# Kernel tuning notes

Hardware: AMD Instinct MI355X
Metric: run time of the kernel (lower is better)

Reference implementation:

```python
import jax, jax.numpy as jnp
import numpy as np

N = 50000       # num_nodes
E = 1_600_000   # num_edges (avg degree 32)
F_IN, HID, F_OUT = 128, 128, 64


def setup_inputs() -> dict:
    key = jax.random.key(0)
    k0, k1, k2, k3 = jax.random.split(key, 4)
    x = jax.random.normal(k0, (1, N, F_IN), dtype=jnp.float32)
    edge_index = jax.random.randint(k1, (2, E), 0, N, dtype=jnp.int32)
    # GCNConv weights (glorot-ish scale) and zero biases
    W1 = jax.random.normal(k2, (F_IN, HID), dtype=jnp.float32) / np.float32(np.sqrt(F_IN))
    b1 = jnp.zeros((HID,), dtype=jnp.float32)
    W2 = jax.random.normal(k3, (HID, F_OUT), dtype=jnp.float32) / np.float32(np.sqrt(HID))
    b2 = jnp.zeros((F_OUT,), dtype=jnp.float32)
    return {"x": x, "edge_index": edge_index, "W1": W1, "b1": b1, "W2": W2, "b2": b2}


def _gcn_layer(h, src, dst, norm, W, b, n):
    # linear transform then symmetric-normalized scatter-add aggregation
    h = h @ W                              # [N, F_out]
    msg = h[src] * norm[:, None]           # [E+N, F_out] gathered messages
    agg = jax.ops.segment_sum(msg, dst, num_segments=n)
    return agg + b


def reference(x, edge_index, W1, b1, W2, b2):
    xn = x[0]                              # [N, F_in] node feature matrix
    n = xn.shape[0]
    src, dst = edge_index[0], edge_index[1]
    # add self-loops (GCNConv default)
    loops = jnp.arange(n, dtype=src.dtype)
    src = jnp.concatenate([src, loops])
    dst = jnp.concatenate([dst, loops])
    # symmetric normalization: deg^-1/2[src] * deg^-1/2[dst] (deg >= 1 w/ self-loops)
    deg = jax.ops.segment_sum(jnp.ones(dst.shape, dtype=xn.dtype), dst, num_segments=n)
    dinv = jax.lax.rsqrt(deg)
    norm = dinv[src] * dinv[dst]
    h = jax.nn.relu(_gcn_layer(xn, src, dst, norm, W1, b1, n))
    out = jax.nn.relu(_gcn_layer(h, src, dst, norm, W2, b2, n))
    return out
```

## Files before the change

### kernel.cpp

```cpp
#include <hip/hip_runtime.h>
#include <hip/hip_fp16.h>


#define TILE 8192
#define BIN_CAP 2560

typedef _Float16 half8 __attribute__((ext_vector_type(8)));
typedef float floatx4 __attribute__((ext_vector_type(4)));

__global__ __launch_bounds__(512) void bin_kernel(const int* __restrict__ src,
                                                  const int* __restrict__ dst, int E,
                                                  int nbins,
                                                  int* __restrict__ binCnt,
                                                  unsigned* __restrict__ recs) {
    extern __shared__ int lds[];
    int* cnt = lds;
    int* gbase = lds + nbins;
    int tid = threadIdx.x;
    for (int i = tid; i < nbins; i += 512) cnt[i] = 0;
    __syncthreads();

    int t0 = blockIdx.x * TILE;
    int tEnd = min(t0 + TILE, E);

    for (int e = t0 + tid; e < tEnd; e += 512)
        atomicAdd(&cnt[dst[e] >> 6], 1);
    __syncthreads();

    for (int i = tid; i < nbins; i += 512) {
        int c = cnt[i];
        gbase[i] = (c > 0) ? atomicAdd(&binCnt[i], c) : 0;
        cnt[i] = 0;
    }
    __syncthreads();

    for (int e = t0 + tid; e < tEnd; e += 512) {
        int d = dst[e];
        int s = src[e];
        int b = d >> 6;
        int r = atomicAdd(&cnt[b], 1);
        int g = gbase[b] + r;
        if (g < BIN_CAP)
            recs[(size_t)b * BIN_CAP + g] = ((unsigned)(d & 63) << 16) | (unsigned)s;
    }
}

__global__ __launch_bounds__(512) void sort_bins(const unsigned* __restrict__ recs,
                                                 const int* __restrict__ binCnt,
                                                 unsigned short* __restrict__ sortedG,
                                                 int* __restrict__ startG,
                                                 float* __restrict__ dinv, int N) {
    __shared__ unsigned short sorted[BIN_CAP];
    __shared__ int c64[64];
    __shared__ int start[65];
    __shared__ int cursor[64];
    int b = blockIdx.x, tid = threadIdx.x;
    int lane = tid & 63, wave = tid >> 6;

    if (tid < 64) c64[tid] = 0;
    __syncthreads();
    int cnt = min(binCnt[b], BIN_CAP);
    const unsigned* bin = recs + (size_t)b * BIN_CAP;

    for (int i = tid; i < cnt; i += 512)
        atomicAdd(&c64[bin[i] >> 16], 1);
    __syncthreads();

    if (wave == 0) {
        int c = c64[lane];
        int v = c;
        #pragma unroll
        for (int off = 1; off < 64; off <<= 1) {
            int t = __shfl_up(v, off);
            if (lane >= off) v += t;
        }
        start[lane] = v - c;
        cursor[lane] = v - c;
        startG[b * 65 + lane] = v - c;
        if (lane == 63) { start[64] = v; startG[b * 65 + 64] = v; }
        int n = (b << 6) + lane;
        if (n < N) dinv[n] = rsqrtf((float)(c + 1));
    }
    __syncthreads();

    for (int i = tid; i < cnt; i += 512) {
        unsigned r = bin[i];
        int pos = atomicAdd(&cursor[r >> 16], 1);
        sorted[pos] = (unsigned short)(r & 0xFFFFu);
    }
    __syncthreads();
    unsigned short* sg = sortedG + (size_t)b * BIN_CAP;
    for (int i = tid; i < cnt; i += 512) sg[i] = sorted[i];
}

template <int COLS, bool FP32IN>
__global__ __launch_bounds__(256) void gemm_mfma(const void* __restrict__ Xv,
                                                 const float* __restrict__ W,
                                                 const float* __restrict__ dinv,
                                                 __half* __restrict__ Y, int N) {
    constexpr int LDA = 136;
    __shared__ __align__(16) _Float16 aT[64 * LDA];
    __shared__ __align__(16) _Float16 bT[COLS * LDA];

    int tid = threadIdx.x;
    int lane = tid & 63, wave = tid >> 6;
    int row0 = blockIdx.x * 64;

    for (int i = tid * 4; i < 64 * 128; i += 1024) {
        int r = i >> 7, k = i & 127;
        int gr = row0 + r;
        if (FP32IN) {
            float4 v = make_float4(0.f, 0.f, 0.f, 0.f);
            if (gr < N) v = *(const float4*)&((const float*)Xv)[(size_t)gr * 128 + k];
            __half2 p0 = __floats2half2_rn(v.x, v.y);
            __half2 p1 = __floats2half2_rn(v.z, v.w);
            *(uint2*)&aT[r * LDA + k] = make_uint2(*(uint*)&p0, *(uint*)&p1);
        } else {
            ushort4 u = make_ushort4(0, 0, 0, 0);
            if (gr < N) u = *(const ushort4*)&((const __half*)Xv)[(size_t)gr * 128 + k];
            *(ushort4*)&aT[r * LDA + k] = u;
        }
    }
    for (int i = tid; i < 128 * COLS; i += 256) {
        int k = i / COLS, n = i % COLS;
        bT[n * LDA + k] = (_Float16)W[i];
    }
    __syncthreads();

    constexpr int NT = COLS / 16;
    floatx4 acc[NT];
    #pragma unroll
    for (int t = 0; t < NT; t++) acc[t] = (floatx4){0.f, 0.f, 0.f, 0.f};

    int m = lane & 15, q = lane >> 4;
    const _Float16* arow = &aT[(wave * 16 + m) * LDA + q * 8];

    #pragma unroll
    for (int ks = 0; ks < 4; ks++) {
        half8 af = *(const half8*)&arow[ks * 32];
        #pragma unroll
        for (int t = 0; t < NT; t++) {
            half8 bf = *(const half8*)&bT[(t * 16 + m) * LDA + ks * 32 + q * 8];
            acc[t] = __builtin_amdgcn_mfma_f32_16x16x32_f16(af, bf, acc[t], 0, 0, 0);
        }
    }
    __syncthreads();

    float dv[4];
    #pragma unroll
    for (int r = 0; r < 4; r++) {
        int gr = row0 + wave * 16 + q * 4 + r;
        dv[r] = (gr < N) ? dinv[gr] : 0.0f;
    }
    #pragma unroll
    for (int t = 0; t < NT; t++)
        #pragma unroll
        for (int r = 0; r < 4; r++)
            aT[(wave * 16 + q * 4 + r) * LDA + t * 16 + m] = (_Float16)(dv[r] * acc[t][r]);
    __syncthreads();

    for (int i = tid; i < 64 * (COLS / 2); i += 256) {
        int r = i / (COLS / 2), c = i % (COLS / 2);
        int gr = row0 + r;
        if (gr < N)
            ((uint*)Y)[(size_t)gr * (COLS / 2) + c] = *(uint*)&aT[r * LDA + c * 2];
    }
}

__global__ __launch_bounds__(512) void agg_gemm_fused(
        const __half* __restrict__ G,
        const unsigned short* __restrict__ sortedG,
        const int* __restrict__ startG,
        const float* __restrict__ dinv,
        const float* __restrict__ bias,
        const float* __restrict__ W2,
        __half* __restrict__ Y2, int N) {
    constexpr int LDH = 136;
    __shared__ unsigned short buf[BIN_CAP];
    __shared__ int st[65];
    __shared__ __align__(16) _Float16 hT[64 * LDH];
    __shared__ __align__(16) _Float16 bT[64 * LDH];

    int b = blockIdx.x;
    int tid = threadIdx.x, lane = tid & 63, wave = tid >> 6;
    int ql = lane & 15, quad = lane >> 4;

    if (tid < 65) st[tid] = startG[b * 65 + tid];
    __syncthreads();
    int cnt = st[64];
    const unsigned short* sg = sortedG + (size_t)b * BIN_CAP;
    for (int i = tid; i < cnt; i += 512) buf[i] = sg[i];
    for (int i = tid; i < 128 * 64; i += 512) {
        int k = i >> 6, n = i & 63;
        bT[n * LDH + k] = (_Float16)W2[i];
    }
    __syncthreads();

    float bb[8];
    #pragma unroll
    for (int k = 0; k < 4; k++) {
        float2 t = *(const float2*)&bias[ql * 8 + k * 2];
        bb[k * 2] = t.x; bb[k * 2 + 1] = t.y;
    }

    for (int rr = 0; rr < 8; rr++) {
        int row = wave * 8 + rr;
        int n = (b << 6) + row;
        if (n >= N) {
            if (quad == 0) {
                uint4 z = make_uint4(0, 0, 0, 0);
                *(uint4*)&hT[row * LDH + ql * 8] = z;
            }
            continue;
        }
        int jst = st[row], jen = st[row + 1];

        float ax[8] = {};
        int j = jst + quad;
        for (; j + 4 < jen; j += 8) {
            int sA = buf[j], sB = buf[j + 4];
            uint4 uA = *(const uint4*)&G[(size_t)sA * 128 + ql * 8];
            uint4 uB = *(const uint4*)&G[(size_t)sB * 128 + ql * 8];
            float2 f;
            f = __half22float2(*(__half2*)&uA.x); ax[0] += f.x; ax[1] += f.y;
            f = __half22float2(*(__half2*)&uA.y); ax[2] += f.x; ax[3] += f.y;
            f = __half22float2(*(__half2*)&uA.z); ax[4] += f.x; ax[5] += f.y;
            f = __half22float2(*(__half2*)&uA.w); ax[6] += f.x; ax[7] += f.y;
            f = __half22float2(*(__half2*)&uB.x); ax[0] += f.x; ax[1] += f.y;
            f = __half22float2(*(__half2*)&uB.y); ax[2] += f.x; ax[3] += f.y;
            f = __half22float2(*(__half2*)&uB.z); ax[4] += f.x; ax[5] += f.y;
            f = __half22float2(*(__half2*)&uB.w); ax[6] += f.x; ax[7] += f.y;
        }
        for (; j < jen; j += 4) {
            int s = buf[j];
            uint4 u = *(const uint4*)&G[(size_t)s * 128 + ql * 8];
            float2 f;
            f = __half22float2(*(__half2*)&u.x); ax[0] += f.x; ax[1] += f.y;
            f = __half22float2(*(__half2*)&u.y); ax[2] += f.x; ax[3] += f.y;
            f = __half22float2(*(__half2*)&u.z); ax[4] += f.x; ax[5] += f.y;
            f = __half22float2(*(__half2*)&u.w); ax[6] += f.x; ax[7] += f.y;
        }
        #pragma unroll
        for (int k = 0; k < 8; k++) {
            ax[k] += __shfl_xor(ax[k], 16);
            ax[k] += __shfl_xor(ax[k], 32);
        }
        if (quad == 0) {
            uint4 us = *(const uint4*)&G[(size_t)n * 128 + ql * 8];
            float2 f;
            f = __half22float2(*(__half2*)&us.x); ax[0] += f.x; ax[1] += f.y;
            f = __half22float2(*(__half2*)&us.y); ax[2] += f.x; ax[3] += f.y;
            f = __half22float2(*(__half2*)&us.z); ax[4] += f.x; ax[5] += f.y;
            f = __half22float2(*(__half2*)&us.w); ax[6] += f.x; ax[7] += f.y;
            float di = dinv[n];
            __half2 h[4];
            #pragma unroll
            for (int k = 0; k < 4; k++) {
                float o0 = fmaxf(fmaf(di, ax[k * 2],     bb[k * 2]),     0.0f);
                float o1 = fmaxf(fmaf(di, ax[k * 2 + 1], bb[k * 2 + 1]), 0.0f);
                h[k] = __floats2half2_rn(o0, o1);
            }
            *(uint4*)&hT[row * LDH + ql * 8] = *(uint4*)h;
        }
    }
    __syncthreads();

    int m = lane & 15, q = lane >> 4;
    int mt = wave & 3, nt0 = (wave >> 2) * 2;
    floatx4 acc[2] = {(floatx4){0.f, 0.f, 0.f, 0.f}, (floatx4){0.f, 0.f, 0.f, 0.f}};
    const _Float16* arow = &hT[(mt * 16 + m) * LDH + q * 8];
    #pragma unroll
    for (int ks = 0; ks < 4; ks++) {
        half8 af = *(const half8*)&arow[ks * 32];
        #pragma unroll
        for (int t = 0; t < 2; t++) {
            half8 bf = *(const half8*)&bT[((nt0 + t) * 16 + m) * LDH + ks * 32 + q * 8];
            acc[t] = __builtin_amdgcn_mfma_f32_16x16x32_f16(af, bf, acc[t], 0, 0, 0);
        }
    }
    __syncthreads();

    float dv[4];
    #pragma unroll
    for (int r = 0; r < 4; r++) {
        int gr = (b << 6) + mt * 16 + q * 4 + r;
        dv[r] = (gr < N) ? dinv[gr] : 0.0f;
    }
    #pragma unroll
    for (int t = 0; t < 2; t++)
        #pragma unroll
        for (int r = 0; r < 4; r++)
            hT[(mt * 16 + q * 4 + r) * LDH + (nt0 + t) * 16 + m] = (_Float16)(dv[r] * acc[t][r]);
    __syncthreads();

    for (int i = tid; i < 64 * 32; i += 512) {
        int r = i >> 5, c = i & 31;
        int gr = (b << 6) + r;
        if (gr < N)
            ((uint*)Y2)[(size_t)gr * 32 + c] = *(uint*)&hT[r * LDH + c * 2];
    }
}

__global__ __launch_bounds__(512) void agg_64(const __half* __restrict__ G,
                                              const unsigned short* __restrict__ sortedG,
                                              const int* __restrict__ startG,
                                              const float* __restrict__ dinv,
                                              const float* __restrict__ bias,
                                              float* __restrict__ out, int N) {
    __shared__ unsigned short buf[BIN_CAP];
    __shared__ int st[33];
    int b = blockIdx.x, half_ = blockIdx.y;
    int tid = threadIdx.x, lane = tid & 63, wave = tid >> 6;
    int ol = lane & 7, oct = lane >> 3;
    int r0 = half_ * 32;

    if (tid < 33) st[tid] = startG[b * 65 + r0 + tid];
    __syncthreads();
    int S0 = st[0], S1 = st[32];
    const unsigned short* sg = sortedG + (size_t)b * BIN_CAP;
    for (int i = tid; i < S1 - S0; i += 512) buf[i] = sg[S0 + i];
    __syncthreads();

    float bb[8];
    #pragma unroll
    for (int k = 0; k < 4; k++) {
        float2 t = *(const float2*)&bias[ol * 8 + k * 2];
        bb[k * 2] = t.x; bb[k * 2 + 1] = t.y;
    }

    for (int rr = 0; rr < 4; rr++) {
        int row = wave * 4 + rr;
        int n = (b << 6) + r0 + row;
        if (n >= N) continue;
        int jst = st[row] - S0, jen = st[row + 1] - S0;

        float ax[8] = {};
        int j = jst + oct;
        for (; j + 8 < jen; j += 16) {
            int sA = buf[j], sB = buf[j + 8];
            uint4 uA = *(const uint4*)&G[(size_t)sA * 64 + ol * 8];
            uint4 uB = *(const uint4*)&G[(size_t)sB * 64 + ol * 8];
            float2 f;
            f = __half22float2(*(__half2*)&uA.x); ax[0] += f.x; ax[1] += f.y;
            f = __half22float2(*(__half2*)&uA.y); ax[2] += f.x; ax[3] += f.y;
            f = __half22float2(*(__half2*)&uA.z); ax[4] += f.x; ax[5] += f.y;
            f = __half22float2(*(__half2*)&uA.w); ax[6] += f.x; ax[7] += f.y;
            f = __half22float2(*(__half2*)&uB.x); ax[0] += f.x; ax[1] += f.y;
            f = __half22float2(*(__half2*)&uB.y); ax[2] += f.x; ax[3] += f.y;
            f = __half22float2(*(__half2*)&uB.z); ax[4] += f.x; ax[5] += f.y;
            f = __half22float2(*(__half2*)&uB.w); ax[6] += f.x; ax[7] += f.y;
        }
        for (; j < jen; j += 8) {
            int s = buf[j];
            uint4 u = *(const uint4*)&G[(size_t)s * 64 + ol * 8];
            float2 f;
            f = __half22float2(*(__half2*)&u.x); ax[0] += f.x; ax[1] += f.y;
            f = __half22float2(*(__half2*)&u.y); ax[2] += f.x; ax[3] += f.y;
            f = __half22float2(*(__half2*)&u.z); ax[4] += f.x; ax[5] += f.y;
            f = __half22float2(*(__half2*)&u.w); ax[6] += f.x; ax[7] += f.y;
        }
        #pragma unroll
        for (int k = 0; k < 8; k++) {
            ax[k] += __shfl_xor(ax[k], 8);
            ax[k] += __shfl_xor(ax[k], 16);
            ax[k] += __shfl_xor(ax[k], 32);
        }
        if (oct < 2) {
            uint4 us = *(const uint4*)&G[(size_t)n * 64 + ol * 8];
            float2 f;
            f = __half22float2(*(__half2*)&us.x); ax[0] += f.x; ax[1] += f.y;
            f = __half22float2(*(__half2*)&us.y); ax[2] += f.x; ax[3] += f.y;
            f = __half22float2(*(__half2*)&us.z); ax[4] += f.x; ax[5] += f.y;
            f = __half22float2(*(__half2*)&us.w); ax[6] += f.x; ax[7] += f.y;
            float di = dinv[n];
            float o[8];
            #pragma unroll
            for (int k = 0; k < 8; k++)
                o[k] = fmaxf(fmaf(di, ax[k], bb[k]), 0.0f);
            if (oct == 0)
                *(float4*)&out[(size_t)n * 64 + ol * 8] = make_float4(o[0], o[1], o[2], o[3]);
            else
                *(float4*)&out[(size_t)n * 64 + ol * 8 + 4] = make_float4(o[4], o[5], o[6], o[7]);
        }
    }
}

extern "C" void kernel_launch(void* const* d_in, const int* in_sizes, int n_in,
                              void* d_out, int out_size, void* d_ws, size_t ws_size,
                              hipStream_t stream) {
    const float* x  = (const float*)d_in[0];
    const int*   ei = (const int*)d_in[1];
    const float* W1 = (const float*)d_in[2];
    const float* b1 = (const float*)d_in[3];
    const float* W2 = (const float*)d_in[4];
    const float* b2 = (const float*)d_in[5];
    float* out = (float*)d_out;

    const int HID  = in_sizes[3];
    const int F_IN = in_sizes[2] / HID;
    const int N    = in_sizes[0] / F_IN;
    const int E    = in_sizes[1] / 2;
    (void)n_in; (void)out_size; (void)ws_size; (void)F_IN;

    const int* src = ei;
    const int* dst = ei + E;

    const int nbins = (N + 63) >> 6;

    char* p = (char*)d_ws;
    auto carve = [&](size_t bytes) { void* q = (void*)p; p += (bytes + 255) & ~(size_t)255; return q; };
    int*            binCnt  = (int*)           carve((size_t)nbins * 4);
    float*          dinv    = (float*)         carve((size_t)N * 4);
    unsigned*       recs    = (unsigned*)      carve((size_t)nbins * BIN_CAP * 4);
    unsigned short* sortedG = (unsigned short*)carve((size_t)nbins * BIN_CAP * 2);
    int*            startG  = (int*)           carve((size_t)nbins * 65 * 4);
    __half*         bufG    = (__half*)        carve((size_t)N * 128 * 2);
    __half*         bufG2   = (__half*)        carve((size_t)N * 64 * 2);

    hipMemsetAsync(binCnt, 0, (size_t)nbins * 4, stream);

    int numTiles = (E + TILE - 1) / TILE;
    size_t binLds = (size_t)nbins * 2 * 4;
    bin_kernel<<<numTiles, 512, binLds, stream>>>(src, dst, E, nbins, binCnt, recs);
    sort_bins<<<nbins, 512, 0, stream>>>(recs, binCnt, sortedG, startG, dinv, N);

    int gemmGrid = (N + 63) / 64;

    gemm_mfma<128, true><<<gemmGrid, 256, 0, stream>>>(x, W1, dinv, bufG, N);

    agg_gemm_fused<<<nbins, 512, 0, stream>>>(bufG, sortedG, startG, dinv, b1, W2, bufG2, N);

    dim3 aggGrid(nbins, 2);
    agg_64<<<aggGrid, 512, 0, stream>>>(bufG2, sortedG, startG, dinv, b2, out, N);
}
```

Measured before the change: 216.4 us.

## Replace bin+sort CSR build with global degree count, prefix, and atomic scatter

The two-pass LDS binning plus per-bin sort is replaced by three kernels: a global per-node degree count with atomics, a per-bin wave prefix scan that writes start offsets, cursors and dinv, and a scatter that places each source index directly at its per-node cursor slot using global atomics. This drops the intermediate 32-bit record buffer and the LDS sort pass, and int4 vectorized loads are used when the inputs are aligned. In exchange it relies on 1.6M contended global atomics on node counters twice, and the order of edges within each node becomes nondeterministic.

```diff
diff --git a/kernel.cpp b/kernel.cpp
--- a/kernel.cpp
+++ b/kernel.cpp
@@ -2,95 +2,94 @@
 #include <hip/hip_fp16.h>
 
 
-#define TILE 8192
 #define BIN_CAP 2560
 
 typedef _Float16 half8 __attribute__((ext_vector_type(8)));
 typedef float floatx4 __attribute__((ext_vector_type(4)));
 
-__global__ __launch_bounds__(512) void bin_kernel(const int* __restrict__ src,
-                                                  const int* __restrict__ dst, int E,
-                                                  int nbins,
-                                                  int* __restrict__ binCnt,
-                                                  unsigned* __restrict__ recs) {
-    extern __shared__ int lds[];
-    int* cnt = lds;
-    int* gbase = lds + nbins;
+template <bool VEC>
+__global__ __launch_bounds__(512) void deg_count(const int* __restrict__ dst, int E,
+                                                 int* __restrict__ deg) {
+    if (VEC) {
+        int i = blockIdx.x * 512 + threadIdx.x;
+        int nv = E >> 2;
+        if (i < nv) {
+            int4 d = ((const int4*)dst)[i];
+            atomicAdd(&deg[d.x], 1);
+            atomicAdd(&deg[d.y], 1);
+            atomicAdd(&deg[d.z], 1);
+            atomicAdd(&deg[d.w], 1);
+        }
+        if (blockIdx.x == 0 && (int)threadIdx.x < (E & 3))
+            atomicAdd(&deg[dst[(nv << 2) + threadIdx.x]], 1);
+    } else {
+        for (int e = blockIdx.x * 512 + threadIdx.x; e < E; e += gridDim.x * 512)
+            atomicAdd(&deg[dst[e]], 1);
+    }
+}
+
+__global__ __launch_bounds__(512) void bin_prefix(const int* __restrict__ deg,
+                                                  int* __restrict__ startG,
+                                                  int* __restrict__ cursor,
+                                                  float* __restrict__ dinv,
+                                                  int N, int nbins) {
     int tid = threadIdx.x;
-    for (int i = tid; i < nbins; i += 512) cnt[i] = 0;
-    __syncthreads();
-
-    int t0 = blockIdx.x * TILE;
-    int tEnd = min(t0 + TILE, E);
-
-    for (int e = t0 + tid; e < tEnd; e += 512)
-        atomicAdd(&cnt[dst[e] >> 6], 1);
-    __syncthreads();
-
-    for (int i = tid; i < nbins; i += 512) {
-        int c = cnt[i];
-        gbase[i] = (c > 0) ? atomicAdd(&binCnt[i], c) : 0;
-        cnt[i] = 0;
-    }
-    __syncthreads();
-
-    for (int e = t0 + tid; e < tEnd; e += 512) {
-        int d = dst[e];
-        int s = src[e];
-        int b = d >> 6;
-        int r = atomicAdd(&cnt[b], 1);
-        int g = gbase[b] + r;
-        if (g < BIN_CAP)
-            recs[(size_t)b * BIN_CAP + g] = ((unsigned)(d & 63) << 16) | (unsigned)s;
-    }
-}
-
-__global__ __launch_bounds__(512) void sort_bins(const unsigned* __restrict__ recs,
-                                                 const int* __restrict__ binCnt,
-                                                 unsigned short* __restrict__ sortedG,
-                                                 int* __restrict__ startG,
-                                                 float* __restrict__ dinv, int N) {
-    __shared__ unsigned short sorted[BIN_CAP];
-    __shared__ int c64[64];
-    __shared__ int start[65];
-    __shared__ int cursor[64];
-    int b = blockIdx.x, tid = threadIdx.x;
     int lane = tid & 63, wave = tid >> 6;
-
-    if (tid < 64) c64[tid] = 0;
-    __syncthreads();
-    int cnt = min(binCnt[b], BIN_CAP);
-    const unsigned* bin = recs + (size_t)b * BIN_CAP;
-
-    for (int i = tid; i < cnt; i += 512)
-        atomicAdd(&c64[bin[i] >> 16], 1);
-    __syncthreads();
-
-    if (wave == 0) {
-        int c = c64[lane];
-        int v = c;
-        #pragma unroll
-        for (int off = 1; off < 64; off <<= 1) {
-            int t = __shfl_up(v, off);
-            if (lane >= off) v += t;
-        }
-        start[lane] = v - c;
-        cursor[lane] = v - c;
-        startG[b * 65 + lane] = v - c;
-        if (lane == 63) { start[64] = v; startG[b * 65 + 64] = v; }
-        int n = (b << 6) + lane;
-        if (n < N) dinv[n] = rsqrtf((float)(c + 1));
-    }
-    __syncthreads();
-
-    for (int i = tid; i < cnt; i += 512) {
-        unsigned r = bin[i];
-        int pos = atomicAdd(&cursor[r >> 16], 1);
-        sorted[pos] = (unsigned short)(r & 0xFFFFu);
-    }
-    __syncthreads();
-    unsigned short* sg = sortedG + (size_t)b * BIN_CAP;
-    for (int i = tid; i < cnt; i += 512) sg[i] = sorted[i];
+    int b = blockIdx.x * 8 + wave;
+    if (b >= nbins) return;
+    int n = (b << 6) + lane;
+    int c = deg[n];
+    int v = c;
+    #pragma unroll
+    for (int off = 1; off < 64; off <<= 1) {
+        int t = __shfl_up(v, off);
+        if (lane >= off) v += t;
+    }
+    int ex = v - c;
+    startG[b * 65 + lane] = min(ex, BIN_CAP);
+    if (lane == 63) startG[b * 65 + 64] = min(v, BIN_CAP);
+    cursor[n] = b * BIN_CAP + ex;
+    if (n < N) dinv[n] = rsqrtf((float)(c + 1));
+}
+
+template <bool VEC>
+__global__ __launch_bounds__(512) void scatter_edges(const int* __restrict__ src,
+                                                     const int* __restrict__ dst, int E,
+                                                     int* __restrict__ cursor,
+                                                     unsigned short* __restrict__ sortedG) {
+    if (VEC) {
+        int i = blockIdx.x * 512 + threadIdx.x;
+        int nv = E >> 2;
+        if (i < nv) {
+            int4 d = ((const int4*)dst)[i];
+            int4 s = ((const int4*)src)[i];
+            int dd[4] = {d.x, d.y, d.z, d.w};
+            int ss[4] = {s.x, s.y, s.z, s.w};
+            #pragma unroll
+            for (int k = 0; k < 4; k++) {
+                int b = dd[k] >> 6;
+                int pos = atomicAdd(&cursor[dd[k]], 1);
+                if (pos - b * BIN_CAP < BIN_CAP)
+                    sortedG[pos] = (unsigned short)ss[k];
+            }
+        }
+        if (blockIdx.x == 0 && (int)threadIdx.x < (E & 3)) {
+            int e = (nv << 2) + threadIdx.x;
+            int dd = dst[e];
+            int b = dd >> 6;
+            int pos = atomicAdd(&cursor[dd], 1);
+            if (pos - b * BIN_CAP < BIN_CAP)
+                sortedG[pos] = (unsigned short)src[e];
+        }
+    } else {
+        for (int e = blockIdx.x * 512 + threadIdx.x; e < E; e += gridDim.x * 512) {
+            int dd = dst[e];
+            int b = dd >> 6;
+            int pos = atomicAdd(&cursor[dd], 1);
+            if (pos - b * BIN_CAP < BIN_CAP)
+                sortedG[pos] = (unsigned short)src[e];
+        }
+    }
 }
 
 template <int COLS, bool FP32IN>
@@ -409,20 +408,32 @@
 
     char* p = (char*)d_ws;
     auto carve = [&](size_t bytes) { void* q = (void*)p; p += (bytes + 255) & ~(size_t)255; return q; };
-    int*            binCnt  = (int*)           carve((size_t)nbins * 4);
+    int*            deg     = (int*)           carve((size_t)nbins * 64 * 4);
+    int*            cursor  = (int*)           carve((size_t)nbins * 64 * 4);
     float*          dinv    = (float*)         carve((size_t)N * 4);
-    unsigned*       recs    = (unsigned*)      carve((size_t)nbins * BIN_CAP * 4);
     unsigned short* sortedG = (unsigned short*)carve((size_t)nbins * BIN_CAP * 2);
     int*            startG  = (int*)           carve((size_t)nbins * 65 * 4);
     __half*         bufG    = (__half*)        carve((size_t)N * 128 * 2);
     __half*         bufG2   = (__half*)        carve((size_t)N * 64 * 2);
 
-    hipMemsetAsync(binCnt, 0, (size_t)nbins * 4, stream);
-
-    int numTiles = (E + TILE - 1) / TILE;
-    size_t binLds = (size_t)nbins * 2 * 4;
-    bin_kernel<<<numTiles, 512, binLds, stream>>>(src, dst, E, nbins, binCnt, recs);
-    sort_bins<<<nbins, 512, 0, stream>>>(recs, binCnt, sortedG, startG, dinv, N);
+    hipMemsetAsync(deg, 0, (size_t)nbins * 64 * 4, stream);
+
+    bool vec = (((reinterpret_cast<uintptr_t>(src) |
+                  reinterpret_cast<uintptr_t>(dst)) & 15) == 0) && (E >= 4);
+    if (vec) {
+        int nv = E >> 2;
+        int pblocks = (nv + 511) / 512;
+        if (pblocks < 1) pblocks = 1;
+        deg_count<true><<<pblocks, 512, 0, stream>>>(dst, E, deg);
+        bin_prefix<<<(nbins + 7) / 8, 512, 0, stream>>>(deg, startG, cursor, dinv, N, nbins);
+        scatter_edges<true><<<pblocks, 512, 0, stream>>>(src, dst, E, cursor, sortedG);
+    } else {
+        int pblocks = min((E + 511) / 512, 2048);
+        if (pblocks < 1) pblocks = 1;
+        deg_count<false><<<pblocks, 512, 0, stream>>>(dst, E, deg);
+        bin_prefix<<<(nbins + 7) / 8, 512, 0, stream>>>(deg, startG, cursor, dinv, N, nbins);
+        scatter_edges<false><<<pblocks, 512, 0, stream>>>(src, dst, E, cursor, sortedG);
+    }
 
     int gemmGrid = (N + 63) / 64;
 
```

After: 365.0 us. 1.69x slower.
